# Performance work log

Measured on AMD Instinct MI355X. Metric: run time of the kernel, lower is better.

Reference implementation:

```python
import jax, jax.numpy as jnp
import numpy as np
import math

DENOM = 32.0

# e3nn scalar_activation normalizes the activation to unit second moment under N(0,1).
# Compute the gelu normalization constant by Gauss-Hermite quadrature.
_zs, _ws = np.polynomial.hermite_e.hermegauss(64)
_g = 0.5 * _zs * (1.0 + np.array([math.erf(z / math.sqrt(2.0)) for z in _zs]))
C_GELU = float(1.0 / math.sqrt((_ws * _g * _g).sum() / math.sqrt(2.0 * math.pi)))


def _spherical_harmonics(r):
    # r: [E,3] unit vectors. Component-normalized real SH for l=1,2,3.
    x, y, z = r[..., 0], r[..., 1], r[..., 2]
    s3, s5, s15 = math.sqrt(3.0), math.sqrt(5.0), math.sqrt(15.0)
    s7, s105 = math.sqrt(7.0), math.sqrt(105.0)
    s35_8, s21_8 = math.sqrt(35.0 / 8.0), math.sqrt(21.0 / 8.0)
    Y1 = s3 * r                                                     # [E,3]
    Y2 = jnp.stack([s15 * x * y, s15 * y * z, 0.5 * s5 * (3 * z * z - 1),
                    s15 * x * z, 0.5 * s15 * (x * x - y * y)], -1)   # [E,5]
    Y3 = jnp.stack([s35_8 * y * (3 * x * x - y * y), s105 * x * y * z,
                    s21_8 * y * (5 * z * z - 1), 0.5 * s7 * z * (5 * z * z - 3),
                    s21_8 * x * (5 * z * z - 1), 0.5 * s105 * z * (x * x - y * y),
                    s35_8 * x * (x * x - 3 * y * y)], -1)            # [E,7]
    return [Y1, Y2, Y3]


def setup_inputs() -> dict:
    key = jax.random.key(0)
    k = jax.random.split(key, 7)
    N, E, MUL, TMUL = 32768, 1048576, 16, 32
    return {
        "x": jax.random.normal(k[0], (N, MUL), jnp.float32),
        "positions": jax.random.normal(k[1], (N, 3), jnp.float32),
        "W_pre": jax.random.normal(k[2], (4, MUL, TMUL), jnp.float32),
        "W_post": jax.random.normal(k[3], (4, TMUL, TMUL), jnp.float32),
        "W_shortcut": jax.random.normal(k[4], (MUL, TMUL), jnp.float32),
        "senders": jax.random.randint(k[5], (E,), 0, N, jnp.int32),
        "receivers": jax.random.randint(k[6], (E,), 0, N, jnp.int32),
    }


def reference(x, positions, W_pre, W_post, W_shortcut, senders, receivers):
    N, mul = x.shape
    tmul = W_pre.shape[-1]
    # --- edge update: sh of relative positions, tensor product with sender scalars ---
    rvec = positions[receivers] - positions[senders]                 # [E,3]
    n = jnp.linalg.norm(rvec, axis=-1, keepdims=True)
    rhat = rvec / jnp.where(n == 0, 1.0, n)
    Ys = _spherical_harmonics(rhat)
    s = x[senders]                                                   # [E,mul] (0e)
    # --- aggregate edge features at receivers (segment sum) ---
    agg = [jax.ops.segment_sum(s, receivers, num_segments=N)]        # 0e block
    for Y in Ys:
        e = (s[:, :, None] * Y[:, None, :]).reshape(s.shape[0], -1)  # 0e x l -> l
        agg.append(jax.ops.segment_sum(e, receivers, num_segments=N).reshape(N, mul, Y.shape[-1]))
    # --- node update: linear_pre -> scalar act -> linear_post, plus shortcut ---
    inv_in = 1.0 / math.sqrt(mul)
    inv_mid = 1.0 / math.sqrt(tmul)
    out = []
    for l in range(4):
        a = agg[l] / DENOM
        if l == 0:
            p = (a @ W_pre[0]) * inv_in
            p = C_GELU * jax.nn.gelu(p, approximate=False)           # act on 0e scalars only
            q = (p @ W_post[0]) * inv_mid
            q = q + (x @ W_shortcut) * inv_in                        # shortcut: only 0e path exists
            out.append(q)
        else:
            p = jnp.einsum('nui,uv->nvi', a, W_pre[l]) * inv_in
            q = jnp.einsum('nvi,vw->nwi', p, W_post[l]) * inv_mid
            out.append(q.reshape(N, -1))
    return jnp.concatenate(out, axis=-1)                              # [N, tmul*16]
```

## Files before the change

### kernel.cpp

```cpp
#include <hip/hip_runtime.h>
#include <math.h>

#define NN 32768
#define EN 1048576
#define NBIN 256
#define BINCAP 8192
#define TILE 4096

#define C_GELU_F 1.5335262f

__global__ __launch_bounds__(256) void bin_k(const int* __restrict__ snd,
                                             const int* __restrict__ rcv,
                                             int* __restrict__ bin_cur,
                                             unsigned* __restrict__ binbuf) {
    __shared__ unsigned cnt[NBIN];
    __shared__ unsigned excl[NBIN];
    __shared__ unsigned cur2[NBIN];
    __shared__ unsigned gbase[NBIN];
    __shared__ unsigned stage[TILE];
    int t = threadIdx.x;
    int tile = blockIdx.x * TILE;
    cnt[t] = 0; cur2[t] = 0;
    __syncthreads();

    unsigned w[TILE / 256];
#pragma unroll
    for (int i = 0; i < TILE / 256; ++i) {
        int e = tile + i * 256 + t;
        unsigned r = (unsigned)rcv[e], s = (unsigned)snd[e];
        w[i] = (r << 15) | s;
        atomicAdd(&cnt[w[i] >> 22], 1u);
    }
    __syncthreads();

    unsigned my = cnt[t];
    excl[t] = my;
    __syncthreads();
    for (int d = 1; d < NBIN; d <<= 1) {
        unsigned v = (t >= d) ? excl[t - d] : 0u;
        __syncthreads();
        excl[t] += v;
        __syncthreads();
    }
    unsigned myexcl = excl[t] - my;
    gbase[t] = atomicAdd((unsigned*)&bin_cur[t], my);
    __syncthreads();
    excl[t] = myexcl;
    __syncthreads();

#pragma unroll
    for (int i = 0; i < TILE / 256; ++i) {
        unsigned b = w[i] >> 22;
        unsigned p = excl[b] + atomicAdd(&cur2[b], 1u);
        stage[p] = w[i];
    }
    __syncthreads();

    for (int p = t; p < TILE; p += 256) {
        unsigned ww = stage[p];
        unsigned b = ww >> 22;
        unsigned idx = gbase[b] + ((unsigned)p - excl[b]);
        if (idx < BINCAP) binbuf[b * BINCAP + idx] = ww;
    }
}

__global__ __launch_bounds__(256) void scan_k(const int* __restrict__ bin_cur,
                                              int* __restrict__ bin_start) {
    __shared__ unsigned sc[NBIN];
    int t = threadIdx.x;
    unsigned my = (unsigned)bin_cur[t];
    sc[t] = my;
    __syncthreads();
    for (int d = 1; d < NBIN; d <<= 1) {
        unsigned v = (t >= d) ? sc[t - d] : 0u;
        __syncthreads();
        sc[t] += v;
        __syncthreads();
    }
    bin_start[t] = (int)(sc[t] - my);
}

__global__ __launch_bounds__(256) void csr_k(const int* __restrict__ bin_cur,
                                             const int* __restrict__ bin_start,
                                             const unsigned* __restrict__ binbuf,
                                             int* __restrict__ row_ptr,
                                             int* __restrict__ edge_csr) {
    __shared__ unsigned cnt[128];
    __shared__ unsigned excl[128];
    __shared__ unsigned cur2[128];
    int b = blockIdx.x;
    int t = threadIdx.x;
    int M = bin_cur[b]; M = M > BINCAP ? BINCAP : M;
    int base = bin_start[b];
    if (t < 128) { cnt[t] = 0; cur2[t] = 0; }
    __syncthreads();

    const unsigned* bb = binbuf + b * BINCAP;
    for (int i = t; i < M; i += 256)
        atomicAdd(&cnt[(bb[i] >> 15) & 127], 1u);
    __syncthreads();

    if (t < 128) excl[t] = cnt[t];
    __syncthreads();
    for (int d = 1; d < 128; d <<= 1) {
        unsigned v = (t >= d && t < 128) ? excl[t - d] : 0u;
        __syncthreads();
        if (t < 128) excl[t] += v;
        __syncthreads();
    }
    if (t < 128) {
        unsigned e = excl[t] - cnt[t];
        excl[t] = e;
        row_ptr[(b << 7) + t] = base + (int)e;
        if (b == NBIN - 1 && t == 127) row_ptr[NN] = base + (int)(e + cnt[127]);
    }
    __syncthreads();

    for (int i = t; i < M; i += 256) {
        unsigned ww = bb[i];
        unsigned r7 = (ww >> 15) & 127;
        unsigned dst = excl[r7] + atomicAdd(&cur2[r7], 1u);
        edge_csr[base + dst] = (int)(ww & 0x7FFF);
    }
}

__global__ __launch_bounds__(256) void pos_k(const float* __restrict__ pos,
                                             float4* __restrict__ posw) {
    int n = blockIdx.x * 256 + threadIdx.x;
    posw[n] = make_float4(pos[3*n], pos[3*n+1], pos[3*n+2], 0.f);
}

__global__ __launch_bounds__(256) void agg_k(const float* __restrict__ x,
                                             const float4* __restrict__ posw,
                                             const int* __restrict__ row_ptr,
                                             const int* __restrict__ edge_csr,
                                             float* __restrict__ agg) {
    int n = blockIdx.x * 16 + (threadIdx.x >> 4);
    int u = threadIdx.x & 15;
    int beg = row_ptr[n], end = row_ptr[n + 1];
    float4 rp = posw[n];
    float acc[16];
#pragma unroll
    for (int j = 0; j < 16; ++j) acc[j] = 0.f;

    const float s3   = 1.7320508075688772f;
    const float s5   = 2.2360679774997896f;
    const float s15  = 3.8729833462074170f;
    const float s7   = 2.6457513110645907f;
    const float s105 = 10.246950765959598f;
    const float s35_8 = 2.0916500663351889f;
    const float s21_8 = 1.6201851746019651f;

    for (int k = beg; k < end; ++k) {
        int s = edge_csr[k];
        float4 sp = posw[s];
        float vx = rp.x - sp.x, vy = rp.y - sp.y, vz = rp.z - sp.z;
        float sv = x[(s << 4) + u];
        float n2 = vx*vx + vy*vy + vz*vz;
        float inv;
        if (n2 > 0.f) {
            inv = rsqrtf(n2);
            inv = inv * (1.5f - 0.5f * n2 * inv * inv);
        } else inv = 0.f;
        float X = vx*inv, Y = vy*inv, Z = vz*inv;
        float XX = X*X, YY = Y*Y, ZZ = Z*Z;

        acc[0]  += sv;
        acc[1]  += sv * (s3*X);
        acc[2]  += sv * (s3*Y);
        acc[3]  += sv * (s3*Z);
        acc[4]  += sv * (s15*X*Y);
        acc[5]  += sv * (s15*Y*Z);
        acc[6]  += sv * (0.5f*s5*(3.f*ZZ - 1.f));
        acc[7]  += sv * (s15*X*Z);
        acc[8]  += sv * (0.5f*s15*(XX - YY));
        acc[9]  += sv * (s35_8*Y*(3.f*XX - YY));
        acc[10] += sv * (s105*X*Y*Z);
        acc[11] += sv * (s21_8*Y*(5.f*ZZ - 1.f));
        acc[12] += sv * (0.5f*s7*Z*(5.f*ZZ - 3.f));
        acc[13] += sv * (s21_8*X*(5.f*ZZ - 1.f));
        acc[14] += sv * (0.5f*s105*Z*(XX - YY));
        acc[15] += sv * (s35_8*X*(XX - 3.f*YY));
    }

    float4* o = (float4*)(agg + (n << 8) + (u << 4));
    o[0] = make_float4(acc[0],  acc[1],  acc[2],  acc[3]);
    o[1] = make_float4(acc[4],  acc[5],  acc[6],  acc[7]);
    o[2] = make_float4(acc[8],  acc[9],  acc[10], acc[11]);
    o[3] = make_float4(acc[12], acc[13], acc[14], acc[15]);
}

__global__ __launch_bounds__(256) void upd_k(const float* __restrict__ x,
                                             const float* __restrict__ Wpre,
                                             const float* __restrict__ Wpost,
                                             const float* __restrict__ Wsc,
                                             const float* __restrict__ agg,
                                             float* __restrict__ out) {
    __shared__ float sPre[4*516];
    __shared__ float sPost[4*1028];
    __shared__ float sSc[512];
    int t = threadIdx.x;
    for (int idx = t; idx < 2048; idx += 256)
        sPre[(idx >> 9)*516 + (idx & 511)] = Wpre[idx];
    for (int idx = t; idx < 4096; idx += 256)
        sPost[(idx >> 10)*1028 + (idx & 1023)] = Wpost[idx];
    sSc[t] = Wsc[t];
    sSc[t + 256] = Wsc[t + 256];
    __syncthreads();

    int n = (blockIdx.x * 256 + t) >> 4;
    int j = t & 15;
    int l, i, offl, deg;
    if (j == 0)      { l = 0; i = 0;     offl = 0;   deg = 1; }
    else if (j < 4)  { l = 1; i = j - 1; offl = 32;  deg = 3; }
    else if (j < 9)  { l = 2; i = j - 4; offl = 128; deg = 5; }
    else             { l = 3; i = j - 9; offl = 288; deg = 7; }

    const float c1 = 0.0078125f;
    const float c2 = 0.17677669529663687f;

    const float* ap = agg + (n << 8) + j;
    float p[32];
#pragma unroll
    for (int v = 0; v < 32; ++v) p[v] = 0.f;
    const float* wp = sPre + l * 516;
#pragma unroll
    for (int u = 0; u < 16; ++u) {
        float a = ap[u << 4];
        const float4* w4 = (const float4*)(wp + (u << 5));
#pragma unroll
        for (int vq = 0; vq < 8; ++vq) {
            float4 w = w4[vq];
            p[4*vq+0] += a * w.x;
            p[4*vq+1] += a * w.y;
            p[4*vq+2] += a * w.z;
            p[4*vq+3] += a * w.w;
        }
    }
#pragma unroll
    for (int v = 0; v < 32; ++v) p[v] *= c1;

    if (j == 0) {
#pragma unroll
        for (int v = 0; v < 32; ++v) {
            float pv = p[v];
            p[v] = C_GELU_F * 0.5f * pv * (1.f + erff(pv * 0.7071067811865476f));
        }
    }

    float q[32];
#pragma unroll
    for (int w = 0; w < 32; ++w) q[w] = 0.f;
    const float* wq = sPost + l * 1028;
#pragma unroll
    for (int v = 0; v < 32; ++v) {
        float pv = p[v];
        const float4* w4 = (const float4*)(wq + (v << 5));
#pragma unroll
        for (int wd = 0; wd < 8; ++wd) {
            float4 w = w4[wd];
            q[4*wd+0] += pv * w.x;
            q[4*wd+1] += pv * w.y;
            q[4*wd+2] += pv * w.z;
            q[4*wd+3] += pv * w.w;
        }
    }
#pragma unroll
    for (int w = 0; w < 32; ++w) q[w] *= c2;

    if (j == 0) {
        const float* xp = x + (n << 4);
#pragma unroll
        for (int u = 0; u < 16; ++u) {
            float xv = 0.25f * xp[u];
            const float4* w4 = (const float4*)(sSc + (u << 5));
#pragma unroll
            for (int wd = 0; wd < 8; ++wd) {
                float4 w = w4[wd];
                q[4*wd+0] += xv * w.x;
                q[4*wd+1] += xv * w.y;
                q[4*wd+2] += xv * w.z;
                q[4*wd+3] += xv * w.w;
            }
        }
    }

    float* op = out + (n << 9) + offl + i;
#pragma unroll
    for (int w = 0; w < 32; ++w) op[w * deg] = q[w];
}

extern "C" void kernel_launch(void* const* d_in, const int* in_sizes, int n_in,
                              void* d_out, int out_size, void* d_ws, size_t ws_size,
                              hipStream_t stream) {
    const float* x     = (const float*)d_in[0];
    const float* pos   = (const float*)d_in[1];
    const float* Wpre  = (const float*)d_in[2];
    const float* Wpost = (const float*)d_in[3];
    const float* Wsc   = (const float*)d_in[4];
    const int*   snd   = (const int*)d_in[5];
    const int*   rcv   = (const int*)d_in[6];
    float* out = (float*)d_out;

    char* ws = (char*)d_ws;
    int*      bin_cur   = (int*)(ws);
    int*      bin_start = (int*)(ws + 1024);
    int*      row_ptr   = (int*)(ws + 2048);
    float4*   posw      = (float4*)(ws + 0x30000);
    int*      edge_csr  = (int*)(ws + 0xB0000);
    unsigned* binbuf    = (unsigned*)(ws + 0x500000);
    float*    agg       = (float*)(ws + 0x1000000);

    hipMemsetAsync(bin_cur, 0, NBIN * sizeof(int), stream);
    bin_k<<<EN / TILE, 256, 0, stream>>>(snd, rcv, bin_cur, binbuf);
    scan_k<<<1, 256, 0, stream>>>(bin_cur, bin_start);
    csr_k<<<NBIN, 256, 0, stream>>>(bin_cur, bin_start, binbuf, row_ptr, edge_csr);
    pos_k<<<NN / 256, 256, 0, stream>>>(pos, posw);
    agg_k<<<NN / 16, 256, 0, stream>>>(x, posw, row_ptr, edge_csr, agg);
    upd_k<<<(NN * 16) / 256, 256, 0, stream>>>(x, Wpre, Wpost, Wsc, agg, out);
}
```

Before: 219.2 us.

## Fuse edge aggregation with node update and software-prefetch neighbor loads

Merges the aggregation and node-update kernels into one kernel. Per-node aggregates are staged in padded shared memory instead of a global agg buffer, which removes the 32 MB write and read-back plus one launch. The edge loop now prefetches the next sender's index, position and feature one iteration ahead to hide gather latency. In exchange, each aggregation block must also load the weight matrices into LDS, and the larger LDS footprint may lower occupancy during the latency-bound gather phase.

Result: slower. 232.5 us (+6.1%).

```diff
diff --git a/kernel.cpp b/kernel.cpp
--- a/kernel.cpp
+++ b/kernel.cpp
@@ -130,14 +130,35 @@
     posw[n] = make_float4(pos[3*n], pos[3*n+1], pos[3*n+2], 0.f);
 }
 
-__global__ __launch_bounds__(256) void agg_k(const float* __restrict__ x,
-                                             const float4* __restrict__ posw,
-                                             const int* __restrict__ row_ptr,
-                                             const int* __restrict__ edge_csr,
-                                             float* __restrict__ agg) {
-    int n = blockIdx.x * 16 + (threadIdx.x >> 4);
-    int u = threadIdx.x & 15;
+#define TSTRIDE 17
+#define NSTRIDE (16 * TSTRIDE)
+
+__global__ __launch_bounds__(256) void fused_k(const float* __restrict__ x,
+                                               const float4* __restrict__ posw,
+                                               const int* __restrict__ row_ptr,
+                                               const int* __restrict__ edge_csr,
+                                               const float* __restrict__ Wpre,
+                                               const float* __restrict__ Wpost,
+                                               const float* __restrict__ Wsc,
+                                               float* __restrict__ out) {
+    __shared__ float sPre[4*516];
+    __shared__ float sPost[4*1028];
+    __shared__ float sSc[512];
+    __shared__ float sT[16 * NSTRIDE];
+
+    int t = threadIdx.x;
+    for (int idx = t; idx < 2048; idx += 256)
+        sPre[(idx >> 9)*516 + (idx & 511)] = Wpre[idx];
+    for (int idx = t; idx < 4096; idx += 256)
+        sPost[(idx >> 10)*1028 + (idx & 1023)] = Wpost[idx];
+    sSc[t] = Wsc[t];
+    sSc[t + 256] = Wsc[t + 256];
+
+    int nl = t >> 4;
+    int n  = blockIdx.x * 16 + nl;
+    int u  = t & 15;
     int beg = row_ptr[n], end = row_ptr[n + 1];
+    int cnt = end - beg;
     float4 rp = posw[n];
     float acc[16];
 #pragma unroll
@@ -151,11 +172,23 @@
     const float s35_8 = 2.0916500663351889f;
     const float s21_8 = 1.6201851746019651f;
 
-    for (int k = beg; k < end; ++k) {
-        int s = edge_csr[k];
-        float4 sp = posw[s];
+    int cl = cnt > 0 ? cnt - 1 : 0;
+    int sA = edge_csr[beg];
+    int sB = edge_csr[beg + (1 < cl ? 1 : cl)];
+    float4 spA = posw[sA];
+    float  xvA = x[(sA << 4) + u];
+
+    for (int k = 0; k < cnt; ++k) {
+        int    s  = sA;
+        float4 sp = spA;
+        float  sv = xvA;
+        sA = sB;
+        int k2 = k + 2; k2 = k2 < cl ? k2 : cl;
+        sB = edge_csr[beg + k2];
+        spA = posw[sA];
+        xvA = x[(sA << 4) + u];
+
         float vx = rp.x - sp.x, vy = rp.y - sp.y, vz = rp.z - sp.z;
-        float sv = x[(s << 4) + u];
         float n2 = vx*vx + vy*vy + vz*vz;
         float inv;
         if (n2 > 0.f) {
@@ -183,32 +216,11 @@
         acc[15] += sv * (s35_8*X*(XX - 3.f*YY));
     }
 
-    float4* o = (float4*)(agg + (n << 8) + (u << 4));
-    o[0] = make_float4(acc[0],  acc[1],  acc[2],  acc[3]);
-    o[1] = make_float4(acc[4],  acc[5],  acc[6],  acc[7]);
-    o[2] = make_float4(acc[8],  acc[9],  acc[10], acc[11]);
-    o[3] = make_float4(acc[12], acc[13], acc[14], acc[15]);
-}
-
-__global__ __launch_bounds__(256) void upd_k(const float* __restrict__ x,
-                                             const float* __restrict__ Wpre,
-                                             const float* __restrict__ Wpost,
-                                             const float* __restrict__ Wsc,
-                                             const float* __restrict__ agg,
-                                             float* __restrict__ out) {
-    __shared__ float sPre[4*516];
-    __shared__ float sPost[4*1028];
-    __shared__ float sSc[512];
-    int t = threadIdx.x;
-    for (int idx = t; idx < 2048; idx += 256)
-        sPre[(idx >> 9)*516 + (idx & 511)] = Wpre[idx];
-    for (int idx = t; idx < 4096; idx += 256)
-        sPost[(idx >> 10)*1028 + (idx & 1023)] = Wpost[idx];
-    sSc[t] = Wsc[t];
-    sSc[t + 256] = Wsc[t + 256];
-    __syncthreads();
-
-    int n = (blockIdx.x * 256 + t) >> 4;
+    float* tp = sT + nl * NSTRIDE + u * TSTRIDE;
+#pragma unroll
+    for (int j = 0; j < 16; ++j) tp[j] = acc[j];
+    __syncthreads();
+
     int j = t & 15;
     int l, i, offl, deg;
     if (j == 0)      { l = 0; i = 0;     offl = 0;   deg = 1; }
@@ -219,15 +231,15 @@
     const float c1 = 0.0078125f;
     const float c2 = 0.17677669529663687f;
 
-    const float* ap = agg + (n << 8) + j;
+    const float* ap = sT + nl * NSTRIDE + j;
     float p[32];
 #pragma unroll
     for (int v = 0; v < 32; ++v) p[v] = 0.f;
     const float* wp = sPre + l * 516;
 #pragma unroll
-    for (int u = 0; u < 16; ++u) {
-        float a = ap[u << 4];
-        const float4* w4 = (const float4*)(wp + (u << 5));
+    for (int uu = 0; uu < 16; ++uu) {
+        float a = ap[uu * TSTRIDE];
+        const float4* w4 = (const float4*)(wp + (uu << 5));
 #pragma unroll
         for (int vq = 0; vq < 8; ++vq) {
             float4 w = w4[vq];
@@ -271,9 +283,9 @@
     if (j == 0) {
         const float* xp = x + (n << 4);
 #pragma unroll
-        for (int u = 0; u < 16; ++u) {
-            float xv = 0.25f * xp[u];
-            const float4* w4 = (const float4*)(sSc + (u << 5));
+        for (int uu = 0; uu < 16; ++uu) {
+            float xv = 0.25f * xp[uu];
+            const float4* w4 = (const float4*)(sSc + (uu << 5));
 #pragma unroll
             for (int wd = 0; wd < 8; ++wd) {
                 float4 w = w4[wd];
@@ -309,13 +321,12 @@
     float4*   posw      = (float4*)(ws + 0x30000);
     int*      edge_csr  = (int*)(ws + 0xB0000);
     unsigned* binbuf    = (unsigned*)(ws + 0x500000);
-    float*    agg       = (float*)(ws + 0x1000000);
 
     hipMemsetAsync(bin_cur, 0, NBIN * sizeof(int), stream);
     bin_k<<<EN / TILE, 256, 0, stream>>>(snd, rcv, bin_cur, binbuf);
     scan_k<<<1, 256, 0, stream>>>(bin_cur, bin_start);
     csr_k<<<NBIN, 256, 0, stream>>>(bin_cur, bin_start, binbuf, row_ptr, edge_csr);
     pos_k<<<NN / 256, 256, 0, stream>>>(pos, posw);
-    agg_k<<<NN / 16, 256, 0, stream>>>(x, posw, row_ptr, edge_csr, agg);
-    upd_k<<<(NN * 16) / 256, 256, 0, stream>>>(x, Wpre, Wpost, Wsc, agg, out);
-}
+    fused_k<<<NN / 16, 256, 0, stream>>>(x, posw, row_ptr, edge_csr,
+                                         Wpre, Wpost, Wsc, out);
+}
```
